# Kernel tuning notes

Hardware: AMD Instinct MI355X
Metric: run time of the kernel (lower is better)

Reference implementation:

```python
import jax, jax.numpy as jnp
import numpy as np

N, D, H, E, K = 65536, 128, 256, 32, 2


def setup_inputs() -> dict:
    key = jax.random.key(0)
    ks = jax.random.split(key, 7)
    s_in = 1.0 / np.sqrt(D)
    s_hid = 1.0 / np.sqrt(H)
    return {
        "x": jax.random.normal(ks[0], (N, D), dtype=jnp.float32),
        "W1": jax.random.uniform(ks[1], (E, D, H), jnp.float32, -s_in, s_in),
        "b1": jax.random.uniform(ks[2], (E, H), jnp.float32, -s_in, s_in),
        "W2": jax.random.uniform(ks[3], (E, H, D), jnp.float32, -s_hid, s_hid),
        "b2": jax.random.uniform(ks[4], (E, D), jnp.float32, -s_hid, s_hid),
        "Wr": jax.random.uniform(ks[5], (D, E), jnp.float32, -s_in, s_in),
        "br": jax.random.uniform(ks[6], (E,), jnp.float32, -s_in, s_in),
    }


def reference(x, W1, b1, W2, b2, Wr, br):
    # Router (eval mode: no gate noise)
    logits = x @ Wr + br                                  # [N, E]
    scores = jax.nn.softmax(logits, axis=-1)              # [N, E]
    topk_vals, topk_inds = jax.lax.top_k(scores, K)       # [N, K]

    # dispatch_mask: zeros scattered with top-k probs (scatter_ on dim 1)
    n = x.shape[0]
    dispatch_mask = jnp.zeros_like(scores).at[
        jnp.arange(n)[:, None], topk_inds
    ].set(topk_vals)                                      # [N, E]

    # Dense all-experts compute, as in the reference torch.stack
    h = jax.nn.relu(jnp.einsum("nd,edh->neh", x, W1) + b1)   # [N, E, H]
    expert_outputs = jnp.einsum("neh,ehd->ned", h, W2) + b2  # [N, E, D]

    output = jnp.einsum("ned,ne->nd", expert_outputs, dispatch_mask)  # [N, D]

    importance = dispatch_mask.sum(axis=0)                # [E]
    imp_mean = jnp.mean(importance)
    imp_var = jnp.var(importance, ddof=1)                 # torch.var is unbiased
    load_balancing_loss = imp_var / (imp_mean ** 2 + 1e-9)
    return output, load_balancing_loss
```

## Files before the change

### kernel.cpp

```cpp
#include <hip/hip_runtime.h>
#include <hip/hip_bf16.h>
#include <cstdint>
#include <cstddef>

#define N_TOK 65536
#define DIM 128
#define HID 256
#define NE 32
#define TOPK 2

typedef __bf16 bf16x8 __attribute__((ext_vector_type(8)));
typedef float f32x4 __attribute__((ext_vector_type(4)));
typedef unsigned uint4v __attribute__((ext_vector_type(4)));

__device__ __forceinline__ unsigned short f2bf(float f) {
  unsigned u = __builtin_bit_cast(unsigned, f);
  u += 0x7fffu + ((u >> 16) & 1u);
  return (unsigned short)(u >> 16);
}
__device__ __forceinline__ float bf2f(unsigned s) {
  return __builtin_bit_cast(float, s << 16);
}
__device__ __forceinline__ uint2 split2(float f0, float f1) {
  unsigned u0 = __builtin_bit_cast(unsigned, f0);
  unsigned u1 = __builtin_bit_cast(unsigned, f1);
  unsigned hi = (u0 >> 16) | (u1 & 0xffff0000u);
  float r0 = f0 - __builtin_bit_cast(float, u0 & 0xffff0000u);
  float r1 = f1 - __builtin_bit_cast(float, u1 & 0xffff0000u);
  unsigned lo = (__builtin_bit_cast(unsigned, r0) >> 16) |
                (__builtin_bit_cast(unsigned, r1) & 0xffff0000u);
  uint2 ret; ret.x = hi; ret.y = lo;
  return ret;
}

__global__ void k_zero_out(float* __restrict__ out) {
  int t = blockIdx.x * 256 + threadIdx.x;
  float4 z = make_float4(0.f, 0.f, 0.f, 0.f);
  float4* o4 = (float4*)out;
  o4[t] = z;
  o4[t + 1048576] = z;
}

__global__ void k_weights(const float* __restrict__ W1, const float* __restrict__ W2,
                          const float* __restrict__ Wr,
                          unsigned short* __restrict__ w1t, unsigned short* __restrict__ w2t,
                          double* __restrict__ wrt64, unsigned short* __restrict__ wrb,
                          float* __restrict__ ws32, int* __restrict__ n_suspect) {
  int b = blockIdx.x;
  if (b == 512) {
    if (threadIdx.x == 0) *n_suspect = 0;
#pragma unroll
    for (int j = 0; j < 16; ++j) {
      int idx = j * 256 + threadIdx.x;
      int e = idx >> 7, d = idx & 127;
      wrt64[idx] = (double)Wr[d * NE + e];
    }
#pragma unroll
    for (int j = 0; j < 16; ++j) {
      int idx = j * 256 + threadIdx.x;
      int k = idx >> 5, e = idx & 31;
      float w = Wr[k * NE + e];
      unsigned u = __builtin_bit_cast(unsigned, w);
      unsigned short hs = (unsigned short)(u >> 16);
      float r = w - __builtin_bit_cast(float, u & 0xffff0000u);
      unsigned short ls = (unsigned short)(__builtin_bit_cast(unsigned, r) >> 16);
      int nt = e >> 4, n = e & 15, kc = k >> 5, q = (k >> 3) & 3, jj = k & 7;
      size_t base = ((((size_t)nt * 4 + kc) * 4 + q) * 16 + n) * 8 + jj;
      wrb[base] = hs;
      wrb[8192 + base] = ls;
    }
    return;
  }
  if (b == 0 && threadIdx.x < 96) ws32[threadIdx.x] = 0.f;
  const float* in;
  unsigned short* out;
  int K, r0, c0;
  if (b < 256) {
    int e = b >> 3, tt = b & 7;
    in = W1 + (size_t)e * DIM * HID;
    out = w1t + (size_t)e * DIM * HID;
    K = HID;
    r0 = (tt >> 2) * 64; c0 = (tt & 3) * 64;
  } else {
    b -= 256;
    int e = b >> 3, tt = b & 7;
    in = W2 + (size_t)e * HID * DIM;
    out = w2t + (size_t)e * HID * DIM;
    K = DIM;
    r0 = (tt >> 1) * 64; c0 = (tt & 1) * 64;
  }
  __shared__ float tile[64][65];
  int t2 = threadIdx.x;
  int r = t2 >> 2, cs = (t2 & 3) * 16;
  const float* src = in + (size_t)(r0 + r) * K + c0 + cs;
#pragma unroll
  for (int j = 0; j < 4; ++j) {
    float4 v = *(const float4*)(src + j * 4);
    tile[r][cs + j * 4 + 0] = v.x;
    tile[r][cs + j * 4 + 1] = v.y;
    tile[r][cs + j * 4 + 2] = v.z;
    tile[r][cs + j * 4 + 3] = v.w;
  }
  __syncthreads();
#pragma unroll
  for (int p = 0; p < 2; ++p) {
    int orow = p * 32 + (t2 >> 3);
    int oc8 = (t2 & 7) * 8;
    int rr = r0 + oc8;
    unsigned pk[4];
#pragma unroll
    for (int q = 0; q < 4; ++q) {
      unsigned lo = f2bf(tile[oc8 + 2 * q][orow]);
      unsigned hi = f2bf(tile[oc8 + 2 * q + 1][orow]);
      pk[q] = lo | (hi << 16);
    }
    uint4 u;
    u.x = pk[0]; u.y = pk[1]; u.z = pk[2]; u.w = pk[3];
    size_t addr = (size_t)(rr >> 5) * (K * 32) + (size_t)(c0 + orow) * 32 + (rr & 31);
    *(uint4*)(out + addr) = u;
  }
}

__global__ __launch_bounds__(256, 2) void k_router(
    const float* __restrict__ x, const unsigned short* __restrict__ wrb,
    const float* __restrict__ br, int* __restrict__ top_idx, float* __restrict__ top_val,
    unsigned short* __restrict__ xb, int* __restrict__ counts,
    float* __restrict__ importance, int* __restrict__ suspects,
    int* __restrict__ n_suspect) {
  __shared__ int hc[NE];
  __shared__ float hf[NE];
  int t = threadIdx.x;
  if (t < NE) { hc[t] = 0; hf[t] = 0.f; }
  __syncthreads();
  int w = t >> 6, l = t & 63, quad = l >> 4, l15 = l & 15;
  int tok0 = blockIdx.x * 128 + w * 32;

  bf16x8 bfr[2][2][4];
#pragma unroll
  for (int s = 0; s < 2; ++s)
#pragma unroll
    for (int nt = 0; nt < 2; ++nt)
#pragma unroll
      for (int kc = 0; kc < 4; ++kc)
        bfr[s][nt][kc] = *(const bf16x8*)(wrb + s * 8192 +
                          ((((size_t)nt * 4 + kc) * 4 + quad) * 16 + l15) * 8);

  f32x4 acc[2][2];
#pragma unroll
  for (int a = 0; a < 2; ++a)
#pragma unroll
    for (int b = 0; b < 2; ++b) {
      f32x4 z = {0.f, 0.f, 0.f, 0.f};
      acc[a][b] = z;
    }

#pragma unroll
  for (int mt = 0; mt < 2; ++mt) {
    const float* xp = x + (size_t)(tok0 + mt * 16 + l15) * DIM + quad * 8;
    float4 va[4][2];
#pragma unroll
    for (int kc = 0; kc < 4; ++kc) {
      const float4* p = (const float4*)(xp + kc * 32);
      va[kc][0] = p[0];
      va[kc][1] = p[1];
    }
    unsigned short* xrow = xb + (size_t)(tok0 + mt * 16 + l15) * DIM + quad * 8;
#pragma unroll
    for (int kc = 0; kc < 4; ++kc) {
      uint4 u;
      u.x = (unsigned)f2bf(va[kc][0].x) | ((unsigned)f2bf(va[kc][0].y) << 16);
      u.y = (unsigned)f2bf(va[kc][0].z) | ((unsigned)f2bf(va[kc][0].w) << 16);
      u.z = (unsigned)f2bf(va[kc][1].x) | ((unsigned)f2bf(va[kc][1].y) << 16);
      u.w = (unsigned)f2bf(va[kc][1].z) | ((unsigned)f2bf(va[kc][1].w) << 16);
      *(uint4*)(xrow + kc * 32) = u;
    }
#pragma unroll
    for (int kc = 0; kc < 4; ++kc) {
      uint2 s0 = split2(va[kc][0].x, va[kc][0].y);
      uint2 s1 = split2(va[kc][0].z, va[kc][0].w);
      uint2 s2 = split2(va[kc][1].x, va[kc][1].y);
      uint2 s3 = split2(va[kc][1].z, va[kc][1].w);
      uint4v hu, lu;
      hu[0] = s0.x; lu[0] = s0.y;
      hu[1] = s1.x; lu[1] = s1.y;
      hu[2] = s2.x; lu[2] = s2.y;
      hu[3] = s3.x; lu[3] = s3.y;
      bf16x8 ahi = __builtin_bit_cast(bf16x8, hu);
      bf16x8 alo = __builtin_bit_cast(bf16x8, lu);
#pragma unroll
      for (int nt = 0; nt < 2; ++nt) {
        acc[mt][nt] = __builtin_amdgcn_mfma_f32_16x16x32_bf16(ahi, bfr[0][nt][kc], acc[mt][nt], 0, 0, 0);
        acc[mt][nt] = __builtin_amdgcn_mfma_f32_16x16x32_bf16(ahi, bfr[1][nt][kc], acc[mt][nt], 0, 0, 0);
        acc[mt][nt] = __builtin_amdgcn_mfma_f32_16x16x32_bf16(alo, bfr[0][nt][kc], acc[mt][nt], 0, 0, 0);
      }
    }
  }

  float brv0 = br[l15], brv1 = br[16 + l15];
  const float NINF = -3.0e38f;
#pragma unroll
  for (int mt = 0; mt < 2; ++mt) {
#pragma unroll
    for (int r = 0; r < 4; ++r) {
      float c0 = acc[mt][0][r] + brv0;
      float c1 = acc[mt][1][r] + brv1;
      float va = (c0 >= c1) ? c0 : c1;
      int ia = (c0 >= c1) ? l15 : 16 + l15;
#pragma unroll
      for (int off = 1; off < 16; off <<= 1) {
        float ov = __shfl_xor(va, off);
        int oi = __shfl_xor(ia, off);
        if (ov > va || (ov == va && oi < ia)) { va = ov; ia = oi; }
      }
      float v1 = va; int i1 = ia;
      float d0 = (i1 == l15) ? NINF : c0;
      float d1 = (i1 == 16 + l15) ? NINF : c1;
      float vb = (d0 >= d1) ? d0 : d1;
      int ib = (d0 >= d1) ? l15 : 16 + l15;
#pragma unroll
      for (int off = 1; off < 16; off <<= 1) {
        float ov = __shfl_xor(vb, off);
        int oi = __shfl_xor(ib, off);
        if (ov > vb || (ov == vb && oi < ib)) { vb = ov; ib = oi; }
      }
      float v2 = vb; int i2 = ib;
      float e0 = (i1 == l15 || i2 == l15) ? NINF : c0;
      float e1 = (i1 == 16 + l15 || i2 == 16 + l15) ? NINF : c1;
      float vc = (e0 >= e1) ? e0 : e1;
#pragma unroll
      for (int off = 1; off < 16; off <<= 1) {
        float ov = __shfl_xor(vc, off);
        vc = (ov > vc) ? ov : vc;
      }
      float s = __expf(c0 - v1) + __expf(c1 - v1);
#pragma unroll
      for (int off = 1; off < 16; off <<= 1) s += __shfl_xor(s, off);
      if (l15 == 0) {
        int n = tok0 + mt * 16 + quad * 4 + r;
        int2 ti; ti.x = i1; ti.y = i2;
        float2 tv; tv.x = 1.0f / s; tv.y = __expf(v2 - v1) / s;
        ((int2*)top_idx)[n] = ti;
        ((float2*)top_val)[n] = tv;
        atomicAdd(&hc[i1], 1);
        atomicAdd(&hc[i2], 1);
        atomicAdd(&hf[i1], tv.x);
        atomicAdd(&hf[i2], tv.y);
        if (v2 - vc < 2e-3f) {
          int sidx = atomicAdd(n_suspect, 1);
          if (sidx < 65536) suspects[sidx] = n;
        }
      }
    }
  }
  __syncthreads();
  if (t < NE) {
    atomicAdd(&counts[t], hc[t]);
    atomicAdd(&importance[t], hf[t]);
  }
}

__global__ __launch_bounds__(256) void k_router_fix(
    const float* __restrict__ x, const double* __restrict__ wrt64,
    const float* __restrict__ br, const int* __restrict__ suspects,
    const int* __restrict__ n_suspect, int* __restrict__ top_idx,
    float* __restrict__ top_val, int* __restrict__ counts,
    float* __restrict__ importance) {
  int t = threadIdx.x;
  int lt = t & 31;
  int gid = blockIdx.x * 8 + (t >> 5);
  int cnt = *n_suspect;
  if (cnt > 65536) cnt = 65536;
  const double* wcol = wrt64 + lt * DIM;
  for (int s = gid; s < cnt; s += 128 * 8) {
    int n = suspects[s];
    const float* xr = x + (size_t)n * DIM;
    double a = 0.0;
#pragma unroll 8
    for (int d = 0; d < DIM; ++d) a = fma((double)xr[d], wcol[d], a);
    double lv = a + (double)br[lt];

    double v1 = lv; int i1 = lt;
#pragma unroll
    for (int off = 16; off > 0; off >>= 1) {
      double ov = __shfl_xor(v1, off, 32);
      int oi = __shfl_xor(i1, off, 32);
      if (ov > v1 || (ov == v1 && oi < i1)) { v1 = ov; i1 = oi; }
    }
    double lv2 = (lt == i1) ? -1.0e300 : lv;
    double v2 = lv2; int i2 = lt;
#pragma unroll
    for (int off = 16; off > 0; off >>= 1) {
      double ov = __shfl_xor(v2, off, 32);
      int oi = __shfl_xor(i2, off, 32);
      if (ov > v2 || (ov == v2 && oi < i2)) { v2 = ov; i2 = oi; }
    }
    float p = expf((float)(lv - v1));
    float ssum = p;
#pragma unroll
    for (int off = 16; off > 0; off >>= 1) ssum += __shfl_xor(ssum, off, 32);
    if (lt == 0) {
      int o1 = top_idx[n * 2 + 0];
      int o2 = top_idx[n * 2 + 1];
      float w1v = top_val[n * 2 + 0];
      float w2v = top_val[n * 2 + 1];
      float nv1 = 1.0f / ssum;
      float nv2 = expf((float)(v2 - v1)) / ssum;
      if (o1 != i1) { atomicAdd(&counts[o1], -1); atomicAdd(&counts[i1], 1); }
      if (o2 != i2) { atomicAdd(&counts[o2], -1); atomicAdd(&counts[i2], 1); }
      atomicAdd(&importance[o1], -w1v);
      atomicAdd(&importance[o2], -w2v);
      atomicAdd(&importance[i1], nv1);
      atomicAdd(&importance[i2], nv2);
      top_idx[n * 2 + 0] = i1;
      top_idx[n * 2 + 1] = i2;
      top_val[n * 2 + 0] = nv1;
      top_val[n * 2 + 1] = nv2;
    }
  }
}

__global__ __launch_bounds__(256) void k_router_f64(const float* __restrict__ x,
                                                    const double* __restrict__ wrt64,
                                                    const float* __restrict__ br,
                                                    int* __restrict__ top_idx,
                                                    float* __restrict__ top_val) {
  int t = threadIdx.x;
  int lt = t & 31;
  int n = blockIdx.x * 8 + (t >> 5);
  const double* wcol = wrt64 + lt * DIM;
  const float* xr = x + (size_t)n * DIM;
  double a = 0.0;
#pragma unroll 8
  for (int d = 0; d < DIM; ++d) a = fma((double)xr[d], wcol[d], a);
  double lv = a + (double)br[lt];
  double v1 = lv; int i1 = lt;
#pragma unroll
  for (int off = 16; off > 0; off >>= 1) {
    double ov = __shfl_xor(v1, off, 32);
    int oi = __shfl_xor(i1, off, 32);
    if (ov > v1 || (ov == v1 && oi < i1)) { v1 = ov; i1 = oi; }
  }
  double lv2 = (lt == i1) ? -1.0e300 : lv;
  double v2 = lv2; int i2 = lt;
#pragma unroll
  for (int off = 16; off > 0; off >>= 1) {
    double ov = __shfl_xor(v2, off, 32);
    int oi = __shfl_xor(i2, off, 32);
    if (ov > v2 || (ov == v2 && oi < i2)) { v2 = ov; i2 = oi; }
  }
  float p = expf((float)(lv - v1));
  float ssum = p;
#pragma unroll
  for (int off = 16; off > 0; off >>= 1) ssum += __shfl_xor(ssum, off, 32);
  if (lt == 0) {
    top_idx[n * 2 + 0] = i1;
    top_idx[n * 2 + 1] = i2;
    top_val[n * 2 + 0] = 1.0f / ssum;
    top_val[n * 2 + 1] = expf((float)(v2 - v1)) / ssum;
  }
}

__global__ void k_hist(const int* __restrict__ top_idx, const float* __restrict__ top_val,
                       int* __restrict__ counts, float* __restrict__ importance) {
  __shared__ int hc[NE];
  __shared__ float hf[NE];
  int t = threadIdx.x;
  if (t < NE) { hc[t] = 0; hf[t] = 0.f; }
  __syncthreads();
#pragma unroll
  for (int j = 0; j < 2; ++j) {
    int i = (j * 256 + blockIdx.x) * 256 + t;
    int e = top_idx[i];
    atomicAdd(&hc[e], 1);
    atomicAdd(&hf[e], top_val[i]);
  }
  __syncthreads();
  if (t < NE) {
    atomicAdd(&counts[t], hc[t]);
    atomicAdd(&importance[t], hf[t]);
  }
}

__global__ void k_scatter(const int* __restrict__ top_idx, const float* __restrict__ top_val,
                          const int* __restrict__ counts, const float* __restrict__ importance,
                          int* __restrict__ cursors, int* __restrict__ perm,
                          float* __restrict__ gatev, int* __restrict__ inv,
                          int* __restrict__ offsets, float* __restrict__ out_loss) {
  __shared__ int hist[NE], base[NE], cur[NE], soff[NE];
  int t = threadIdx.x;
  if (t < NE) { hist[t] = 0; cur[t] = 0; }
  if (t < 32) {
    int pc = (counts[t] + 63) & ~63;
    int sc = pc;
#pragma unroll
    for (int off = 1; off < 32; off <<= 1) {
      int ov = __shfl_up(sc, off, 32);
      if (t >= off) sc += ov;
    }
    soff[t] = sc - pc;
    if (blockIdx.x == 0) {
      offsets[t] = sc - pc;
      if (t == 31) offsets[NE] = sc;
      float imp = importance[t];
      float ssum = imp;
#pragma unroll
      for (int off = 16; off > 0; off >>= 1) ssum += __shfl_xor(ssum, off, 32);
      float mean = ssum / 32.0f;
      float dlt = imp - mean;
      float v = dlt * dlt;
#pragma unroll
      for (int off = 16; off > 0; off >>= 1) v += __shfl_xor(v, off, 32);
      if (t == 0) *out_loss = (v / 31.0f) / (mean * mean + 1e-9f);
    }
  }
  __syncthreads();
#pragma unroll
  for (int j = 0; j < 4; ++j) {
    int i = blockIdx.x * 1024 + j * 256 + t;
    atomicAdd(&hist[top_idx[i]], 1);
  }
  __syncthreads();
  if (t < NE) base[t] = atomicAdd(&cursors[t], hist[t]);
  __syncthreads();
#pragma unroll
  for (int j = 0; j < 4; ++j) {
    int i = blockIdx.x * 1024 + j * 256 + t;
    int e = top_idx[i];
    int p = atomicAdd(&cur[e], 1);
    int pos = soff[e] + base[e] + p;
    perm[pos] = i >> 1;
    gatev[pos] = top_val[i];
    inv[i] = pos;
  }
}

template <int YB>
__global__ __launch_bounds__(256, 3) void k_expert(
    const float* __restrict__ x, const unsigned short* __restrict__ xb,
    const unsigned short* __restrict__ w1t, const unsigned short* __restrict__ w2t,
    const float* __restrict__ b1, const float* __restrict__ b2,
    const int* __restrict__ offsets, const int* __restrict__ counts,
    const int* __restrict__ perm, const float* __restrict__ gatev,
    unsigned short* __restrict__ ybuf, float* __restrict__ out) {
  __shared__ __align__(16) unsigned char smem[49152];
  unsigned char* xa = smem;
  unsigned char* ha = smem + 16384;

  int bid = (int)(blockIdx.x & 7) * 260 + (int)(blockIdx.x >> 3);
  int slot0 = bid * 64;
  if (slot0 >= offsets[NE]) return;
  int e = 0;
#pragma unroll
  for (int i = 1; i < NE; ++i)
    if (slot0 >= offsets[i]) e = i;
  int cnt = counts[e];
  int local0 = slot0 - offsets[e];
  int nvalid = min(64, cnt - local0);

  int t = threadIdx.x;
  int w = t >> 6;
  int l = t & 63;
  int quad = l >> 4;
  int l15 = l & 15;

  if (YB) {
    uint4 v[4];
    if (l < nvalid) {
      const uint4* rowp = (const uint4*)(xb + (size_t)perm[slot0 + l] * DIM);
#pragma unroll
      for (int cc = 0; cc < 4; ++cc) v[cc] = rowp[w * 4 + cc];
    } else {
#pragma unroll
      for (int cc = 0; cc < 4; ++cc) { v[cc].x = 0u; v[cc].y = 0u; v[cc].z = 0u; v[cc].w = 0u; }
    }
#pragma unroll
    for (int cc = 0; cc < 4; ++cc)
      *(uint4*)(xa + (size_t)(w * 4 + cc) * 1024 + l * 16) = v[cc];
  } else {
    int r = t & 63;
    int half = t >> 6;
    unsigned pk[16];
    if (r < nvalid) {
      int token = perm[slot0 + r];
      const float* src = x + (size_t)token * DIM + half * 32;
#pragma unroll
      for (int q = 0; q < 8; ++q) {
        float4 vv = ((const float4*)src)[q];
        pk[q * 2 + 0] = (unsigned)f2bf(vv.x) | ((unsigned)f2bf(vv.y) << 16);
        pk[q * 2 + 1] = (unsigned)f2bf(vv.z) | ((unsigned)f2bf(vv.w) << 16);
      }
    } else {
#pragma unroll
      for (int q = 0; q < 16; ++q) pk[q] = 0u;
    }
#pragma unroll
    for (int cc = 0; cc < 4; ++cc) {
      uint4 u;
      u.x = pk[cc * 4 + 0]; u.y = pk[cc * 4 + 1]; u.z = pk[cc * 4 + 2]; u.w = pk[cc * 4 + 3];
      *(uint4*)(xa + (half * 4 + cc) * 1024 + r * 16) = u;
    }
  }

  const unsigned short* w1e = w1t + (size_t)e * DIM * HID;
  bf16x8 w1f[4][4];
#pragma unroll
  for (int kc = 0; kc < 4; ++kc)
#pragma unroll
    for (int jt = 0; jt < 4; ++jt)
      w1f[kc][jt] = *(const bf16x8*)(w1e + kc * 8192 + (w * 64 + jt * 16 + l15) * 32 + quad * 8);

  float gvl = (l < nvalid) ? gatev[slot0 + l] : 0.f;

  __syncthreads();

  f32x4 acc[4][4];
#pragma unroll
  for (int a = 0; a < 4; ++a)
#pragma unroll
    for (int b = 0; b < 4; ++b) {
      f32x4 z = {0.f, 0.f, 0.f, 0.f};
      acc[a][b] = z;
    }
#pragma unroll
  for (int kc = 0; kc < 4; ++kc) {
    bf16x8 af[4];
#pragma unroll
    for (int rt = 0; rt < 4; ++rt)
      af[rt] = *(const bf16x8*)(xa + (kc * 4 + quad) * 1024 + (rt * 16 + l15) * 16);
#pragma unroll
    for (int rt = 0; rt < 4; ++rt)
#pragma unroll
      for (int jt = 0; jt < 4; ++jt)
        acc[rt][jt] = __builtin_amdgcn_mfma_f32_16x16x32_bf16(af[rt], w1f[kc][jt], acc[rt][jt], 0, 0, 0);
  }

  const unsigned short* w2e = w2t + (size_t)e * HID * DIM;
  bf16x8 w2f[8][2];
#pragma unroll
  for (int hc = 0; hc < 8; ++hc)
#pragma unroll
    for (int jt = 0; jt < 2; ++jt)
      w2f[hc][jt] = *(const bf16x8*)(w2e + hc * 4096 + (w * 32 + jt * 16 + l15) * 32 + quad * 8);

  const float* b1e = b1 + e * HID;
#pragma unroll
  for (int jt = 0; jt < 4; ++jt) {
    int col = w * 64 + jt * 16 + l15;
    float b1v = b1e[col];
    int c = col >> 3;
    int byteoff = (col & 7) * 2;
#pragma unroll
    for (int rt = 0; rt < 4; ++rt) {
#pragma unroll
      for (int r = 0; r < 4; ++r) {
        int tokrow = rt * 16 + quad * 4 + r;
        float v = acc[rt][jt][r] + b1v;
        v = v > 0.f ? v : 0.f;
        *(unsigned short*)(ha + c * 1024 + tokrow * 16 + byteoff) = f2bf(v);
      }
    }
  }
  __syncthreads();

  f32x4 accc[4][2];
#pragma unroll
  for (int a = 0; a < 4; ++a)
#pragma unroll
    for (int b = 0; b < 2; ++b) {
      f32x4 z = {0.f, 0.f, 0.f, 0.f};
      accc[a][b] = z;
    }
#pragma unroll
  for (int hc = 0; hc < 8; ++hc) {
    bf16x8 ah[4];
#pragma unroll
    for (int rt = 0; rt < 4; ++rt)
      ah[rt] = *(const bf16x8*)(ha + (hc * 4 + quad) * 1024 + (rt * 16 + l15) * 16);
#pragma unroll
    for (int rt = 0; rt < 4; ++rt)
#pragma unroll
      for (int jt = 0; jt < 2; ++jt)
        accc[rt][jt] = __builtin_amdgcn_mfma_f32_16x16x32_bf16(ah[rt], w2f[hc][jt], accc[rt][jt], 0, 0, 0);
  }

  int dbase = w * 32;
  float b2v0 = b2[e * DIM + dbase + l15];
  float b2v1 = b2[e * DIM + dbase + 16 + l15];
#pragma unroll
  for (int rt = 0; rt < 4; ++rt) {
#pragma unroll
    for (int r = 0; r < 4; ++r) {
      int tokrow = rt * 16 + quad * 4 + r;
      float g = __shfl(gvl, tokrow);
      if (tokrow < nvalid) {
        int pos = slot0 + tokrow;
        if (YB) {
          unsigned short* yrow = ybuf + (size_t)pos * DIM + dbase;
          yrow[l15] = f2bf(g * (accc[rt][0][r] + b2v0));
          yrow[16 + l15] = f2bf(g * (accc[rt][1][r] + b2v1));
        } else {
          int token = perm[pos];
          float* orow = out + (size_t)token * DIM + dbase;
          atomicAdd(&orow[l15], g * (accc[rt][0][r] + b2v0));
          atomicAdd(&orow[16 + l15], g * (accc[rt][1][r] + b2v1));
        }
      }
    }
  }
}

__global__ __launch_bounds__(256) void k_combine(const unsigned short* __restrict__ ybuf,
                                                 const int* __restrict__ inv,
                                                 float* __restrict__ out) {
  int t = threadIdx.x;
  int n = blockIdx.x * 16 + (t >> 4);
  int lane = t & 15;
  int p0 = inv[n * 2 + 0];
  int p1 = inv[n * 2 + 1];
  uint4 a = *((const uint4*)(ybuf + (size_t)p0 * DIM) + lane);
  uint4 b = *((const uint4*)(ybuf + (size_t)p1 * DIM) + lane);
  unsigned av[4] = {a.x, a.y, a.z, a.w}, bv[4] = {b.x, b.y, b.z, b.w};
  float r[8];
#pragma unroll
  for (int q = 0; q < 4; ++q) {
    r[q * 2 + 0] = bf2f(av[q] & 0xffffu) + bf2f(bv[q] & 0xffffu);
    r[q * 2 + 1] = bf2f(av[q] >> 16) + bf2f(bv[q] >> 16);
  }
  float* orow = out + (size_t)n * DIM + lane * 8;
  float4 w0 = {r[0], r[1], r[2], r[3]}, w1 = {r[4], r[5], r[6], r[7]};
  ((float4*)orow)[0] = w0;
  ((float4*)orow)[1] = w1;
}

extern "C" void kernel_launch(void* const* d_in, const int* in_sizes, int n_in,
                              void* d_out, int out_size, void* d_ws, size_t ws_size,
                              hipStream_t stream) {
  const float* x  = (const float*)d_in[0];
  const float* W1 = (const float*)d_in[1];
  const float* b1 = (const float*)d_in[2];
  const float* W2 = (const float*)d_in[3];
  const float* b2 = (const float*)d_in[4];
  const float* Wr = (const float*)d_in[5];
  const float* br = (const float*)d_in[6];
  float* out = (float*)d_out;

  char* ws = (char*)d_ws;
  float* importance   = (float*)(ws + 0);
  int*   counts       = (int*)(ws + 128);
  int*   cursors      = (int*)(ws + 256);
  int*   offsets      = (int*)(ws + 384);
  int*   top_idx      = (int*)(ws + 1024);
  float* top_val      = (float*)(ws + 525312);
  int*   perm         = (int*)(ws + 1049600);
  float* gatev        = (float*)(ws + 1582080);
  int*   inv          = (int*)(ws + 2114560);
  unsigned short* w1t = (unsigned short*)(ws + 2638848);
  unsigned short* w2t = (unsigned short*)(ws + 4736000);
  unsigned short* ybuf = (unsigned short*)(ws + 6833152);
  double* wrt64 = (double*)(ws + 6833152);
  unsigned short* wrb = (unsigned short*)(ws + 6833152 + 32768);
  int* suspects = (int*)(ws + 40911872);
  int* n_suspect = (int*)(ws + 41174016);
  const size_t NEEDED = 41174144;
  bool use_ybuf = ws_size >= NEEDED;

  unsigned short* xb = (unsigned short*)out;

  hipLaunchKernelGGL(k_weights, dim3(513), dim3(256), 0, stream, W1, W2, Wr, w1t, w2t, wrt64,
                     wrb, (float*)ws, n_suspect);
  if (use_ybuf) {
    hipLaunchKernelGGL(k_router, dim3(512), dim3(256), 0, stream, x, wrb, br, top_idx, top_val,
                       xb, counts, importance, suspects, n_suspect);
    hipLaunchKernelGGL(k_router_fix, dim3(128), dim3(256), 0, stream, x, wrt64, br, suspects,
                       n_suspect, top_idx, top_val, counts, importance);
    hipLaunchKernelGGL(k_scatter, dim3(128), dim3(256), 0, stream, top_idx, top_val, counts,
                       importance, cursors, perm, gatev, inv, offsets,
                       out + (size_t)N_TOK * DIM);
    hipLaunchKernelGGL((k_expert<1>), dim3(2080), dim3(256), 0, stream, x, xb, w1t, w2t, b1, b2,
                       offsets, counts, perm, gatev, ybuf, out);
    hipLaunchKernelGGL(k_combine, dim3(4096), dim3(256), 0, stream, ybuf, inv, out);
  } else {
    hipLaunchKernelGGL(k_router_f64, dim3(8192), dim3(256), 0, stream, x, wrt64, br, top_idx,
                       top_val);
    hipLaunchKernelGGL(k_hist, dim3(256), dim3(256), 0, stream, top_idx, top_val, counts,
                       importance);
    hipLaunchKernelGGL(k_scatter, dim3(128), dim3(256), 0, stream, top_idx, top_val, counts,
                       importance, cursors, perm, gatev, inv, offsets,
                       out + (size_t)N_TOK * DIM);
    hipLaunchKernelGGL(k_zero_out, dim3(4096), dim3(256), 0, stream, out);
    hipLaunchKernelGGL((k_expert<0>), dim3(2080), dim3(256), 0, stream, x,
                       (const unsigned short*)0, w1t, w2t, b1, b2, offsets, counts, perm, gatev,
                       ybuf, out);
  }
}
```

Before: 208.7 us.

## Fuse router, weight prep and fix-up into one front kernel; deterministic scatter

Merges weight transposition, router GEMM and the fp64 suspect fix-up into a single front kernel that writes per-block histograms. The old atomic cursors are replaced by a prefix-sum scatter, and the expert kernel now writes outputs directly at each token's slot, so the inverse map is no longer needed. The expert kernel also drops to 32KB of shared memory with an XOR-swizzled LDS layout, gets a higher occupancy bound, and uses vectorized bias loads. This cuts launch count and global atomics. In exchange, the scatter kernel re-reads histograms redundantly in every block, and the fix-up list is capped at 128 per block.

```diff
diff --git a/kernel.cpp b/kernel.cpp
--- a/kernel.cpp
+++ b/kernel.cpp
@@ -12,6 +12,8 @@
 typedef __bf16 bf16x8 __attribute__((ext_vector_type(8)));
 typedef float f32x4 __attribute__((ext_vector_type(4)));
 typedef unsigned uint4v __attribute__((ext_vector_type(4)));
+
+#define LDSA(c, row, byte) ((((c) * 1024 + (row) * 16 + (byte))) ^ ((((c) & 3) << 5)))
 
 __device__ __forceinline__ unsigned short f2bf(float f) {
   unsigned u = __builtin_bit_cast(unsigned, f);
@@ -41,117 +43,114 @@
   o4[t + 1048576] = z;
 }
 
-__global__ void k_weights(const float* __restrict__ W1, const float* __restrict__ W2,
-                          const float* __restrict__ Wr,
-                          unsigned short* __restrict__ w1t, unsigned short* __restrict__ w2t,
-                          double* __restrict__ wrt64, unsigned short* __restrict__ wrb,
-                          float* __restrict__ ws32, int* __restrict__ n_suspect) {
+__global__ __launch_bounds__(256, 2) void k_front(
+    const float* __restrict__ x, const float* __restrict__ W1,
+    const float* __restrict__ W2, const float* __restrict__ Wr,
+    const float* __restrict__ br,
+    int* __restrict__ top_idx, float* __restrict__ top_val,
+    unsigned short* __restrict__ xb,
+    unsigned short* __restrict__ w1t, unsigned short* __restrict__ w2t,
+    int* __restrict__ histbuf, float* __restrict__ impbuf) {
   int b = blockIdx.x;
-  if (b == 512) {
-    if (threadIdx.x == 0) *n_suspect = 0;
-#pragma unroll
-    for (int j = 0; j < 16; ++j) {
-      int idx = j * 256 + threadIdx.x;
-      int e = idx >> 7, d = idx & 127;
-      wrt64[idx] = (double)Wr[d * NE + e];
-    }
-#pragma unroll
-    for (int j = 0; j < 16; ++j) {
-      int idx = j * 256 + threadIdx.x;
-      int k = idx >> 5, e = idx & 31;
-      float w = Wr[k * NE + e];
-      unsigned u = __builtin_bit_cast(unsigned, w);
-      unsigned short hs = (unsigned short)(u >> 16);
-      float r = w - __builtin_bit_cast(float, u & 0xffff0000u);
-      unsigned short ls = (unsigned short)(__builtin_bit_cast(unsigned, r) >> 16);
-      int nt = e >> 4, n = e & 15, kc = k >> 5, q = (k >> 3) & 3, jj = k & 7;
-      size_t base = ((((size_t)nt * 4 + kc) * 4 + q) * 16 + n) * 8 + jj;
-      wrb[base] = hs;
-      wrb[8192 + base] = ls;
+  int t = threadIdx.x;
+
+  if (b >= 512) {
+    int bb = b - 512;
+    const float* in;
+    unsigned short* outp;
+    int K, r0, c0;
+    bool isW1;
+    if (bb < 256) {
+      int e = bb >> 3, tt = bb & 7;
+      in = W1 + (size_t)e * DIM * HID;
+      outp = w1t + (size_t)e * DIM * HID;
+      K = HID;
+      r0 = (tt >> 2) * 64; c0 = (tt & 3) * 64;
+      isW1 = true;
+    } else {
+      bb -= 256;
+      int e = bb >> 3, tt = bb & 7;
+      in = W2 + (size_t)e * HID * DIM;
+      outp = w2t + (size_t)e * HID * DIM;
+      K = DIM;
+      r0 = (tt >> 1) * 64; c0 = (tt & 1) * 64;
+      isW1 = false;
+    }
+    __shared__ float tile[64][65];
+    int r = t >> 2, cs = (t & 3) * 16;
+    const float* src = in + (size_t)(r0 + r) * K + c0 + cs;
+#pragma unroll
+    for (int j = 0; j < 4; ++j) {
+      float4 v = *(const float4*)(src + j * 4);
+      tile[r][cs + j * 4 + 0] = v.x;
+      tile[r][cs + j * 4 + 1] = v.y;
+      tile[r][cs + j * 4 + 2] = v.z;
+      tile[r][cs + j * 4 + 3] = v.w;
+    }
+    __syncthreads();
+#pragma unroll
+    for (int p = 0; p < 2; ++p) {
+      int orow = p * 32 + (t >> 3);
+      int oc8 = (t & 7) * 8;
+      int rr = r0 + oc8;
+      unsigned pk[4];
+#pragma unroll
+      for (int q = 0; q < 4; ++q) {
+        unsigned lo = f2bf(tile[oc8 + 2 * q][orow]);
+        unsigned hi = f2bf(tile[oc8 + 2 * q + 1][orow]);
+        pk[q] = lo | (hi << 16);
+      }
+      uint4 u;
+      u.x = pk[0]; u.y = pk[1]; u.z = pk[2]; u.w = pk[3];
+      int h = c0 + orow;
+      int hp = isW1 ? ((h & ~63) | ((h & 3) << 4) | ((h & 63) >> 2))
+                    : ((h & ~31) | ((h & 1) << 4) | ((h & 31) >> 1));
+      size_t addr = (size_t)(rr >> 5) * (K * 32) + (size_t)hp * 32 + (rr & 31);
+      *(uint4*)(outp + addr) = u;
     }
     return;
   }
-  if (b == 0 && threadIdx.x < 96) ws32[threadIdx.x] = 0.f;
-  const float* in;
-  unsigned short* out;
-  int K, r0, c0;
-  if (b < 256) {
-    int e = b >> 3, tt = b & 7;
-    in = W1 + (size_t)e * DIM * HID;
-    out = w1t + (size_t)e * DIM * HID;
-    K = HID;
-    r0 = (tt >> 2) * 64; c0 = (tt & 3) * 64;
-  } else {
-    b -= 256;
-    int e = b >> 3, tt = b & 7;
-    in = W2 + (size_t)e * HID * DIM;
-    out = w2t + (size_t)e * HID * DIM;
-    K = DIM;
-    r0 = (tt >> 1) * 64; c0 = (tt & 1) * 64;
-  }
-  __shared__ float tile[64][65];
-  int t2 = threadIdx.x;
-  int r = t2 >> 2, cs = (t2 & 3) * 16;
-  const float* src = in + (size_t)(r0 + r) * K + c0 + cs;
-#pragma unroll
-  for (int j = 0; j < 4; ++j) {
-    float4 v = *(const float4*)(src + j * 4);
-    tile[r][cs + j * 4 + 0] = v.x;
-    tile[r][cs + j * 4 + 1] = v.y;
-    tile[r][cs + j * 4 + 2] = v.z;
-    tile[r][cs + j * 4 + 3] = v.w;
-  }
-  __syncthreads();
-#pragma unroll
-  for (int p = 0; p < 2; ++p) {
-    int orow = p * 32 + (t2 >> 3);
-    int oc8 = (t2 & 7) * 8;
-    int rr = r0 + oc8;
-    unsigned pk[4];
-#pragma unroll
-    for (int q = 0; q < 4; ++q) {
-      unsigned lo = f2bf(tile[oc8 + 2 * q][orow]);
-      unsigned hi = f2bf(tile[oc8 + 2 * q + 1][orow]);
-      pk[q] = lo | (hi << 16);
-    }
-    uint4 u;
-    u.x = pk[0]; u.y = pk[1]; u.z = pk[2]; u.w = pk[3];
-    size_t addr = (size_t)(rr >> 5) * (K * 32) + (size_t)(c0 + orow) * 32 + (rr & 31);
-    *(uint4*)(out + addr) = u;
-  }
-}
-
-__global__ __launch_bounds__(256, 2) void k_router(
-    const float* __restrict__ x, const unsigned short* __restrict__ wrb,
-    const float* __restrict__ br, int* __restrict__ top_idx, float* __restrict__ top_val,
-    unsigned short* __restrict__ xb, int* __restrict__ counts,
-    float* __restrict__ importance, int* __restrict__ suspects,
-    int* __restrict__ n_suspect) {
+
   __shared__ int hc[NE];
   __shared__ float hf[NE];
-  int t = threadIdx.x;
+  __shared__ int slist[128];
+  __shared__ int scount;
   if (t < NE) { hc[t] = 0; hf[t] = 0.f; }
-  __syncthreads();
+  if (t == 0) scount = 0;
+  __syncthreads();
+
   int w = t >> 6, l = t & 63, quad = l >> 4, l15 = l & 15;
-  int tok0 = blockIdx.x * 128 + w * 32;
+  int tok0 = b * 128 + w * 32;
 
   bf16x8 bfr[2][2][4];
 #pragma unroll
-  for (int s = 0; s < 2; ++s)
-#pragma unroll
-    for (int nt = 0; nt < 2; ++nt)
-#pragma unroll
-      for (int kc = 0; kc < 4; ++kc)
-        bfr[s][nt][kc] = *(const bf16x8*)(wrb + s * 8192 +
-                          ((((size_t)nt * 4 + kc) * 4 + quad) * 16 + l15) * 8);
+  for (int nt = 0; nt < 2; ++nt)
+#pragma unroll
+    for (int kc = 0; kc < 4; ++kc) {
+      unsigned hiw[4], low[4];
+#pragma unroll
+      for (int jp = 0; jp < 4; ++jp) {
+        int k0 = kc * 32 + quad * 8 + jp * 2;
+        int e = nt * 16 + l15;
+        float w0 = Wr[k0 * NE + e];
+        float w1v = Wr[(k0 + 1) * NE + e];
+        uint2 s = split2(w0, w1v);
+        hiw[jp] = s.x; low[jp] = s.y;
+      }
+      uint4v h4, l4;
+      h4[0] = hiw[0]; h4[1] = hiw[1]; h4[2] = hiw[2]; h4[3] = hiw[3];
+      l4[0] = low[0]; l4[1] = low[1]; l4[2] = low[2]; l4[3] = low[3];
+      bfr[0][nt][kc] = __builtin_bit_cast(bf16x8, h4);
+      bfr[1][nt][kc] = __builtin_bit_cast(bf16x8, l4);
+    }
 
   f32x4 acc[2][2];
 #pragma unroll
   for (int a = 0; a < 2; ++a)
 #pragma unroll
-    for (int b = 0; b < 2; ++b) {
+    for (int bb = 0; bb < 2; ++bb) {
       f32x4 z = {0.f, 0.f, 0.f, 0.f};
-      acc[a][b] = z;
+      acc[a][bb] = z;
     }
 
 #pragma unroll
@@ -246,37 +245,22 @@
         atomicAdd(&hf[i1], tv.x);
         atomicAdd(&hf[i2], tv.y);
         if (v2 - vc < 2e-3f) {
-          int sidx = atomicAdd(n_suspect, 1);
-          if (sidx < 65536) suspects[sidx] = n;
+          int si = atomicAdd(&scount, 1);
+          if (si < 128) slist[si] = n;
         }
       }
     }
   }
   __syncthreads();
-  if (t < NE) {
-    atomicAdd(&counts[t], hc[t]);
-    atomicAdd(&importance[t], hf[t]);
-  }
-}
-
-__global__ __launch_bounds__(256) void k_router_fix(
-    const float* __restrict__ x, const double* __restrict__ wrt64,
-    const float* __restrict__ br, const int* __restrict__ suspects,
-    const int* __restrict__ n_suspect, int* __restrict__ top_idx,
-    float* __restrict__ top_val, int* __restrict__ counts,
-    float* __restrict__ importance) {
-  int t = threadIdx.x;
-  int lt = t & 31;
-  int gid = blockIdx.x * 8 + (t >> 5);
-  int cnt = *n_suspect;
-  if (cnt > 65536) cnt = 65536;
-  const double* wcol = wrt64 + lt * DIM;
-  for (int s = gid; s < cnt; s += 128 * 8) {
-    int n = suspects[s];
+
+  int sc = scount;
+  for (int s = (t >> 5); s < sc; s += 8) {
+    int lt = t & 31;
+    int n = slist[s];
     const float* xr = x + (size_t)n * DIM;
     double a = 0.0;
 #pragma unroll 8
-    for (int d = 0; d < DIM; ++d) a = fma((double)xr[d], wcol[d], a);
+    for (int d = 0; d < DIM; ++d) a = fma((double)xr[d], (double)Wr[d * NE + lt], a);
     double lv = a + (double)br[lt];
 
     double v1 = lv; int i1 = lt;
@@ -305,103 +289,86 @@
       float w2v = top_val[n * 2 + 1];
       float nv1 = 1.0f / ssum;
       float nv2 = expf((float)(v2 - v1)) / ssum;
-      if (o1 != i1) { atomicAdd(&counts[o1], -1); atomicAdd(&counts[i1], 1); }
-      if (o2 != i2) { atomicAdd(&counts[o2], -1); atomicAdd(&counts[i2], 1); }
-      atomicAdd(&importance[o1], -w1v);
-      atomicAdd(&importance[o2], -w2v);
-      atomicAdd(&importance[i1], nv1);
-      atomicAdd(&importance[i2], nv2);
+      atomicAdd(&hc[o1], -1); atomicAdd(&hc[o2], -1);
+      atomicAdd(&hc[i1], 1);  atomicAdd(&hc[i2], 1);
+      atomicAdd(&hf[o1], -w1v); atomicAdd(&hf[o2], -w2v);
+      atomicAdd(&hf[i1], nv1);  atomicAdd(&hf[i2], nv2);
       top_idx[n * 2 + 0] = i1;
       top_idx[n * 2 + 1] = i2;
       top_val[n * 2 + 0] = nv1;
       top_val[n * 2 + 1] = nv2;
     }
   }
-}
-
-__global__ __launch_bounds__(256) void k_router_f64(const float* __restrict__ x,
-                                                    const double* __restrict__ wrt64,
-                                                    const float* __restrict__ br,
-                                                    int* __restrict__ top_idx,
-                                                    float* __restrict__ top_val) {
-  int t = threadIdx.x;
-  int lt = t & 31;
-  int n = blockIdx.x * 8 + (t >> 5);
-  const double* wcol = wrt64 + lt * DIM;
-  const float* xr = x + (size_t)n * DIM;
-  double a = 0.0;
-#pragma unroll 8
-  for (int d = 0; d < DIM; ++d) a = fma((double)xr[d], wcol[d], a);
-  double lv = a + (double)br[lt];
-  double v1 = lv; int i1 = lt;
-#pragma unroll
-  for (int off = 16; off > 0; off >>= 1) {
-    double ov = __shfl_xor(v1, off, 32);
-    int oi = __shfl_xor(i1, off, 32);
-    if (ov > v1 || (ov == v1 && oi < i1)) { v1 = ov; i1 = oi; }
-  }
-  double lv2 = (lt == i1) ? -1.0e300 : lv;
-  double v2 = lv2; int i2 = lt;
-#pragma unroll
-  for (int off = 16; off > 0; off >>= 1) {
-    double ov = __shfl_xor(v2, off, 32);
-    int oi = __shfl_xor(i2, off, 32);
-    if (ov > v2 || (ov == v2 && oi < i2)) { v2 = ov; i2 = oi; }
-  }
-  float p = expf((float)(lv - v1));
-  float ssum = p;
-#pragma unroll
-  for (int off = 16; off > 0; off >>= 1) ssum += __shfl_xor(ssum, off, 32);
-  if (lt == 0) {
-    top_idx[n * 2 + 0] = i1;
-    top_idx[n * 2 + 1] = i2;
-    top_val[n * 2 + 0] = 1.0f / ssum;
-    top_val[n * 2 + 1] = expf((float)(v2 - v1)) / ssum;
-  }
-}
-
-__global__ void k_hist(const int* __restrict__ top_idx, const float* __restrict__ top_val,
-                       int* __restrict__ counts, float* __restrict__ importance) {
-  __shared__ int hc[NE];
-  __shared__ float hf[NE];
-  int t = threadIdx.x;
-  if (t < NE) { hc[t] = 0; hf[t] = 0.f; }
-  __syncthreads();
-#pragma unroll
-  for (int j = 0; j < 2; ++j) {
-    int i = (j * 256 + blockIdx.x) * 256 + t;
-    int e = top_idx[i];
-    atomicAdd(&hc[e], 1);
-    atomicAdd(&hf[e], top_val[i]);
-  }
   __syncthreads();
   if (t < NE) {
-    atomicAdd(&counts[t], hc[t]);
-    atomicAdd(&importance[t], hf[t]);
-  }
-}
-
-__global__ void k_scatter(const int* __restrict__ top_idx, const float* __restrict__ top_val,
-                          const int* __restrict__ counts, const float* __restrict__ importance,
-                          int* __restrict__ cursors, int* __restrict__ perm,
-                          float* __restrict__ gatev, int* __restrict__ inv,
-                          int* __restrict__ offsets, float* __restrict__ out_loss) {
-  __shared__ int hist[NE], base[NE], cur[NE], soff[NE];
-  int t = threadIdx.x;
-  if (t < NE) { hist[t] = 0; cur[t] = 0; }
+    histbuf[b * NE + t] = hc[t];
+    impbuf[b * NE + t] = hf[t];
+  }
+}
+
+__global__ __launch_bounds__(256) void k_scatter2(
+    const int* __restrict__ top_idx, const float* __restrict__ top_val,
+    const int* __restrict__ histbuf, const float* __restrict__ impbuf,
+    int* __restrict__ perm, float* __restrict__ gatev,
+    int* __restrict__ offsets, int* __restrict__ counts, float* __restrict__ out_loss) {
+  __shared__ int pf[8][32], pb[8][32];
+  __shared__ int offs[NE], pref[NE], h2[NE];
+  int b = blockIdx.x, t = threadIdx.x;
+  if (t < NE) h2[t] = 0;
+  int g = t >> 5, e = t & 31;
+  int sf = 0, sb = 0;
+  for (int j = 0; j < 64; ++j) {
+    int bb = g * 64 + j;
+    int v = histbuf[bb * NE + e];
+    sf += v;
+    sb += (bb < b) ? v : 0;
+  }
+  pf[g][e] = sf;
+  pb[g][e] = sb;
+  __syncthreads();
   if (t < 32) {
-    int pc = (counts[t] + 63) & ~63;
-    int sc = pc;
+    int T = 0, P = 0;
+#pragma unroll
+    for (int g2 = 0; g2 < 8; ++g2) { T += pf[g2][t]; P += pb[g2][t]; }
+    int pc = (T + 63) & ~63;
+    int scn = pc;
 #pragma unroll
     for (int off = 1; off < 32; off <<= 1) {
-      int ov = __shfl_up(sc, off, 32);
-      if (t >= off) sc += ov;
-    }
-    soff[t] = sc - pc;
-    if (blockIdx.x == 0) {
-      offsets[t] = sc - pc;
-      if (t == 31) offsets[NE] = sc;
-      float imp = importance[t];
+      int ov = __shfl_up(scn, off, 32);
+      if (t >= off) scn += ov;
+    }
+    offs[t] = scn - pc;
+    pref[t] = P;
+    if (b == 0) {
+      offsets[t] = scn - pc;
+      counts[t] = T;
+      if (t == 31) offsets[NE] = scn;
+    }
+  }
+  __syncthreads();
+  if (t < 128) {
+    int n = b * 128 + t;
+    int2 ti = ((const int2*)top_idx)[n];
+    float2 tv = ((const float2*)top_val)[n];
+    int r0 = atomicAdd(&h2[ti.x], 1);
+    int r1 = atomicAdd(&h2[ti.y], 1);
+    int p0 = offs[ti.x] + pref[ti.x] + r0;
+    int p1 = offs[ti.y] + pref[ti.y] + r1;
+    perm[p0] = n * 2;
+    gatev[p0] = tv.x;
+    perm[p1] = n * 2 + 1;
+    gatev[p1] = tv.y;
+  }
+  if (b == 0) {
+    __shared__ float pfi[8][32];
+    float s2 = 0.f;
+    for (int j = 0; j < 64; ++j) s2 += impbuf[(g * 64 + j) * NE + e];
+    pfi[g][e] = s2;
+    __syncthreads();
+    if (t < 32) {
+      float imp = 0.f;
+#pragma unroll
+      for (int g2 = 0; g2 < 8; ++g2) imp += pfi[g2][t];
       float ssum = imp;
 #pragma unroll
       for (int off = 16; off > 0; off >>= 1) ssum += __shfl_xor(ssum, off, 32);
@@ -413,38 +380,17 @@
       if (t == 0) *out_loss = (v / 31.0f) / (mean * mean + 1e-9f);
     }
   }
-  __syncthreads();
-#pragma unroll
-  for (int j = 0; j < 4; ++j) {
-    int i = blockIdx.x * 1024 + j * 256 + t;
-    atomicAdd(&hist[top_idx[i]], 1);
-  }
-  __syncthreads();
-  if (t < NE) base[t] = atomicAdd(&cursors[t], hist[t]);
-  __syncthreads();
-#pragma unroll
-  for (int j = 0; j < 4; ++j) {
-    int i = blockIdx.x * 1024 + j * 256 + t;
-    int e = top_idx[i];
-    int p = atomicAdd(&cur[e], 1);
-    int pos = soff[e] + base[e] + p;
-    perm[pos] = i >> 1;
-    gatev[pos] = top_val[i];
-    inv[i] = pos;
-  }
 }
 
 template <int YB>
-__global__ __launch_bounds__(256, 3) void k_expert(
+__global__ __launch_bounds__(256, 4) void k_expert(
     const float* __restrict__ x, const unsigned short* __restrict__ xb,
     const unsigned short* __restrict__ w1t, const unsigned short* __restrict__ w2t,
     const float* __restrict__ b1, const float* __restrict__ b2,
     const int* __restrict__ offsets, const int* __restrict__ counts,
     const int* __restrict__ perm, const float* __restrict__ gatev,
-    unsigned short* __restrict__ ybuf, float* __restrict__ out) {
-  __shared__ __align__(16) unsigned char smem[49152];
-  unsigned char* xa = smem;
-  unsigned char* ha = smem + 16384;
+    unsigned short* __restrict__ ybt, float* __restrict__ out) {
+  __shared__ __align__(16) unsigned char smem[32768];
 
   int bid = (int)(blockIdx.x & 7) * 260 + (int)(blockIdx.x >> 3);
   int slot0 = bid * 64;
@@ -463,10 +409,14 @@
   int quad = l >> 4;
   int l15 = l & 15;
 
+  int pvl = 0;
+  float gvl = 0.f;
   if (YB) {
     uint4 v[4];
     if (l < nvalid) {
-      const uint4* rowp = (const uint4*)(xb + (size_t)perm[slot0 + l] * DIM);
+      pvl = perm[slot0 + l];
+      gvl = gatev[slot0 + l];
+      const uint4* rowp = (const uint4*)(xb + (size_t)(pvl >> 1) * DIM);
 #pragma unroll
       for (int cc = 0; cc < 4; ++cc) v[cc] = rowp[w * 4 + cc];
     } else {
@@ -475,14 +425,13 @@
     }
 #pragma unroll
     for (int cc = 0; cc < 4; ++cc)
-      *(uint4*)(xa + (size_t)(w * 4 + cc) * 1024 + l * 16) = v[cc];
+      *(uint4*)(smem + LDSA(w * 4 + cc, l, 0)) = v[cc];
   } else {
-    int r = t & 63;
-    int half = t >> 6;
     unsigned pk[16];
-    if (r < nvalid) {
-      int token = perm[slot0 + r];
-      const float* src = x + (size_t)token * DIM + half * 32;
+    if (l < nvalid) {
+      pvl = perm[slot0 + l];
+      gvl = gatev[slot0 + l];
+      const float* src = x + (size_t)(pvl >> 1) * DIM + w * 32;
 #pragma unroll
       for (int q = 0; q < 8; ++q) {
         float4 vv = ((const float4*)src)[q];
@@ -497,7 +446,7 @@
     for (int cc = 0; cc < 4; ++cc) {
       uint4 u;
       u.x = pk[cc * 4 + 0]; u.y = pk[cc * 4 + 1]; u.z = pk[cc * 4 + 2]; u.w = pk[cc * 4 + 3];
-      *(uint4*)(xa + (half * 4 + cc) * 1024 + r * 16) = u;
+      *(uint4*)(smem + LDSA(w * 4 + cc, l, 0)) = u;
     }
   }
 
@@ -509,24 +458,22 @@
     for (int jt = 0; jt < 4; ++jt)
       w1f[kc][jt] = *(const bf16x8*)(w1e + kc * 8192 + (w * 64 + jt * 16 + l15) * 32 + quad * 8);
 
-  float gvl = (l < nvalid) ? gatev[slot0 + l] : 0.f;
-
   __syncthreads();
 
   f32x4 acc[4][4];
 #pragma unroll
   for (int a = 0; a < 4; ++a)
 #pragma unroll
-    for (int b = 0; b < 4; ++b) {
+    for (int bb = 0; bb < 4; ++bb) {
       f32x4 z = {0.f, 0.f, 0.f, 0.f};
-      acc[a][b] = z;
+      acc[a][bb] = z;
     }
 #pragma unroll
   for (int kc = 0; kc < 4; ++kc) {
     bf16x8 af[4];
 #pragma unroll
     for (int rt = 0; rt < 4; ++rt)
-      af[rt] = *(const bf16x8*)(xa + (kc * 4 + quad) * 1024 + (rt * 16 + l15) * 16);
+      af[rt] = *(const bf16x8*)(smem + LDSA(kc * 4 + quad, rt * 16 + l15, 0));
 #pragma unroll
     for (int rt = 0; rt < 4; ++rt)
 #pragma unroll
@@ -542,21 +489,25 @@
     for (int jt = 0; jt < 2; ++jt)
       w2f[hc][jt] = *(const bf16x8*)(w2e + hc * 4096 + (w * 32 + jt * 16 + l15) * 32 + quad * 8);
 
-  const float* b1e = b1 + e * HID;
-#pragma unroll
-  for (int jt = 0; jt < 4; ++jt) {
-    int col = w * 64 + jt * 16 + l15;
-    float b1v = b1e[col];
-    int c = col >> 3;
-    int byteoff = (col & 7) * 2;
+  __syncthreads();
+
+  {
+    float4 b1v = *(const float4*)(b1 + e * HID + w * 64 + 4 * l15);
+    int c = w * 8 + (l15 >> 1);
+    int byte = (l15 & 1) * 8;
 #pragma unroll
     for (int rt = 0; rt < 4; ++rt) {
 #pragma unroll
       for (int r = 0; r < 4; ++r) {
         int tokrow = rt * 16 + quad * 4 + r;
-        float v = acc[rt][jt][r] + b1v;
-        v = v > 0.f ? v : 0.f;
-        *(unsigned short*)(ha + c * 1024 + tokrow * 16 + byteoff) = f2bf(v);
+        float v0 = acc[rt][0][r] + b1v.x; v0 = v0 > 0.f ? v0 : 0.f;
+        float v1 = acc[rt][1][r] + b1v.y; v1 = v1 > 0.f ? v1 : 0.f;
+        float v2 = acc[rt][2][r] + b1v.z; v2 = v2 > 0.f ? v2 : 0.f;
+        float v3 = acc[rt][3][r] + b1v.w; v3 = v3 > 0.f ? v3 : 0.f;
+        uint2 u;
+        u.x = (unsigned)f2bf(v0) | ((unsigned)f2bf(v1) << 16);
+        u.y = (unsigned)f2bf(v2) | ((unsigned)f2bf(v3) << 16);
+        *(uint2*)(smem + LDSA(c, tokrow, byte)) = u;
       }
     }
   }
@@ -566,16 +517,16 @@
 #pragma unroll
   for (int a = 0; a < 4; ++a)
 #pragma unroll
-    for (int b = 0; b < 2; ++b) {
+    for (int bb = 0; bb < 2; ++bb) {
       f32x4 z = {0.f, 0.f, 0.f, 0.f};
-      accc[a][b] = z;
+      accc[a][bb] = z;
     }
 #pragma unroll
   for (int hc = 0; hc < 8; ++hc) {
     bf16x8 ah[4];
 #pragma unroll
     for (int rt = 0; rt < 4; ++rt)
-      ah[rt] = *(const bf16x8*)(ha + (hc * 4 + quad) * 1024 + (rt * 16 + l15) * 16);
+      ah[rt] = *(const bf16x8*)(smem + LDSA(hc * 4 + quad, rt * 16 + l15, 0));
 #pragma unroll
     for (int rt = 0; rt < 4; ++rt)
 #pragma unroll
@@ -584,41 +535,37 @@
   }
 
   int dbase = w * 32;
-  float b2v0 = b2[e * DIM + dbase + l15];
-  float b2v1 = b2[e * DIM + dbase + 16 + l15];
+  float2 b2v = *(const float2*)(b2 + e * DIM + dbase + 2 * l15);
 #pragma unroll
   for (int rt = 0; rt < 4; ++rt) {
 #pragma unroll
     for (int r = 0; r < 4; ++r) {
       int tokrow = rt * 16 + quad * 4 + r;
+      int pv = __shfl(pvl, tokrow);
       float g = __shfl(gvl, tokrow);
       if (tokrow < nvalid) {
-        int pos = slot0 + tokrow;
+        float y0 = g * (accc[rt][0][r] + b2v.x);
+        float y1 = g * (accc[rt][1][r] + b2v.y);
         if (YB) {
-          unsigned short* yrow = ybuf + (size_t)pos * DIM + dbase;
-          yrow[l15] = f2bf(g * (accc[rt][0][r] + b2v0));
-          yrow[16 + l15] = f2bf(g * (accc[rt][1][r] + b2v1));
+          unsigned pack = (unsigned)f2bf(y0) | ((unsigned)f2bf(y1) << 16);
+          *(unsigned*)(ybt + (size_t)pv * DIM + dbase + 2 * l15) = pack;
         } else {
-          int token = perm[pos];
-          float* orow = out + (size_t)token * DIM + dbase;
-          atomicAdd(&orow[l15], g * (accc[rt][0][r] + b2v0));
-          atomicAdd(&orow[16 + l15], g * (accc[rt][1][r] + b2v1));
+          float* orow = out + (size_t)(pv >> 1) * DIM + dbase + 2 * l15;
+          atomicAdd(&orow[0], y0);
+          atomicAdd(&orow[1], y1);
         }
       }
     }
   }
 }
 
-__global__ __launch_bounds__(256) void k_combine(const unsigned short* __restrict__ ybuf,
-                                                 const int* __restrict__ inv,
+__global__ __launch_bounds__(256) void k_combine(const unsigned short* __restrict__ ybt,
                                                  float* __restrict__ out) {
-  int t = threadIdx.x;
-  int n = blockIdx.x * 16 + (t >> 4);
-  int lane = t & 15;
-  int p0 = inv[n * 2 + 0];
-  int p1 = inv[n * 2 + 1];
-  uint4 a = *((const uint4*)(ybuf + (size_t)p0 * DIM) + lane);
-  uint4 b = *((const uint4*)(ybuf + (size_t)p1 * DIM) + lane);
+  int idx = blockIdx.x * 256 + threadIdx.x;
+  int n = idx >> 4;
+  int lane = idx & 15;
+  uint4 a = *((const uint4*)(ybt + (size_t)(2 * n) * DIM) + lane);
+  uint4 b = *((const uint4*)(ybt + (size_t)(2 * n + 1) * DIM) + lane);
   unsigned av[4] = {a.x, a.y, a.z, a.w}, bv[4] = {b.x, b.y, b.z, b.w};
   float r[8];
 #pragma unroll
@@ -645,51 +592,40 @@
   float* out = (float*)d_out;
 
   char* ws = (char*)d_ws;
-  float* importance   = (float*)(ws + 0);
-  int*   counts       = (int*)(ws + 128);
-  int*   cursors      = (int*)(ws + 256);
-  int*   offsets      = (int*)(ws + 384);
-  int*   top_idx      = (int*)(ws + 1024);
-  float* top_val      = (float*)(ws + 525312);
-  int*   perm         = (int*)(ws + 1049600);
-  float* gatev        = (float*)(ws + 1582080);
-  int*   inv          = (int*)(ws + 2114560);
+  int*   counts   = (int*)(ws + 0);
+  int*   offsets  = (int*)(ws + 128);
+  int*   top_idx  = (int*)(ws + 1024);
+  float* top_val  = (float*)(ws + 525312);
+  int*   perm     = (int*)(ws + 1049600);
+  float* gatev    = (float*)(ws + 1582080);
+  int*   histbuf  = (int*)(ws + 2114560);
+  float* impbuf   = (float*)(ws + 2180096);
   unsigned short* w1t = (unsigned short*)(ws + 2638848);
   unsigned short* w2t = (unsigned short*)(ws + 4736000);
-  unsigned short* ybuf = (unsigned short*)(ws + 6833152);
-  double* wrt64 = (double*)(ws + 6833152);
-  unsigned short* wrb = (unsigned short*)(ws + 6833152 + 32768);
-  int* suspects = (int*)(ws + 40911872);
-  int* n_suspect = (int*)(ws + 41174016);
-  const size_t NEEDED = 41174144;
-  bool use_ybuf = ws_size >= NEEDED;
+  unsigned short* ybt = (unsigned short*)(ws + 6833152);
+  const size_t NEEDED = 40387584;
+  bool use_ybt = ws_size >= NEEDED;
 
   unsigned short* xb = (unsigned short*)out;
 
-  hipLaunchKernelGGL(k_weights, dim3(513), dim3(256), 0, stream, W1, W2, Wr, w1t, w2t, wrt64,
-                     wrb, (float*)ws, n_suspect);
-  if (use_ybuf) {
-    hipLaunchKernelGGL(k_router, dim3(512), dim3(256), 0, stream, x, wrb, br, top_idx, top_val,
-                       xb, counts, importance, suspects, n_suspect);
-    hipLaunchKernelGGL(k_router_fix, dim3(128), dim3(256), 0, stream, x, wrt64, br, suspects,
-                       n_suspect, top_idx, top_val, counts, importance);
-    hipLaunchKernelGGL(k_scatter, dim3(128), dim3(256), 0, stream, top_idx, top_val, counts,
-                       importance, cursors, perm, gatev, inv, offsets,
+  if (use_ybt) {
+    hipLaunchKernelGGL(k_front, dim3(1024), dim3(256), 0, stream, x, W1, W2, Wr, br,
+                       top_idx, top_val, xb, w1t, w2t, histbuf, impbuf);
+    hipLaunchKernelGGL(k_scatter2, dim3(512), dim3(256), 0, stream, top_idx, top_val,
+                       histbuf, impbuf, perm, gatev, offsets, counts,
                        out + (size_t)N_TOK * DIM);
-    hipLaunchKernelGGL((k_expert<1>), dim3(2080), dim3(256), 0, stream, x, xb, w1t, w2t, b1, b2,
-                       offsets, counts, perm, gatev, ybuf, out);
-    hipLaunchKernelGGL(k_combine, dim3(4096), dim3(256), 0, stream, ybuf, inv, out);
+    hipLaunchKernelGGL((k_expert<1>), dim3(2080), dim3(256), 0, stream, x, xb, w1t, w2t,
+                       b1, b2, offsets, counts, perm, gatev, ybt, out);
+    hipLaunchKernelGGL(k_combine, dim3(4096), dim3(256), 0, stream, ybt, out);
   } else {
-    hipLaunchKernelGGL(k_router_f64, dim3(8192), dim3(256), 0, stream, x, wrt64, br, top_idx,
-                       top_val);
-    hipLaunchKernelGGL(k_hist, dim3(256), dim3(256), 0, stream, top_idx, top_val, counts,
-                       importance);
-    hipLaunchKernelGGL(k_scatter, dim3(128), dim3(256), 0, stream, top_idx, top_val, counts,
-                       importance, cursors, perm, gatev, inv, offsets,
+    hipLaunchKernelGGL(k_front, dim3(1024), dim3(256), 0, stream, x, W1, W2, Wr, br,
+                       top_idx, top_val, xb, w1t, w2t, histbuf, impbuf);
+    hipLaunchKernelGGL(k_scatter2, dim3(512), dim3(256), 0, stream, top_idx, top_val,
+                       histbuf, impbuf, perm, gatev, offsets, counts,
                        out + (size_t)N_TOK * DIM);
     hipLaunchKernelGGL(k_zero_out, dim3(4096), dim3(256), 0, stream, out);
     hipLaunchKernelGGL((k_expert<0>), dim3(2080), dim3(256), 0, stream, x,
-                       (const unsigned short*)0, w1t, w2t, b1, b2, offsets, counts, perm, gatev,
-                       ybuf, out);
-  }
-}
+                       (const unsigned short*)0, w1t, w2t, b1, b2, offsets, counts,
+                       perm, gatev, (unsigned short*)0, out);
+  }
+}
```

New measurement: 217.7 us. 1.04x slower.
